# Optimization experiments

Hardware: AMD Instinct MI355X
Metric: run time of the kernel (lower is better)

The kernel has to match this reference:

```python
import jax, jax.numpy as jnp
import numpy as np

HEADS = 16
D_MODEL = 1024
D_K = D_MODEL // HEADS
B, S = 2, 2048
NEG = -1000000000.0


def setup_inputs() -> dict:
    key = jax.random.key(0)
    ks = jax.random.split(key, 8)
    q = jax.random.normal(ks[0], (B, S, D_MODEL), dtype=jnp.float32)
    k = jax.random.normal(ks[1], (B, S, D_MODEL), dtype=jnp.float32)
    v = jax.random.normal(ks[2], (B, S, D_MODEL), dtype=jnp.float32)
    mask = jax.random.randint(ks[3], (B, 1, S, S), 0, 2) > 0  # True = masked
    scale = 1.0 / np.sqrt(D_MODEL)
    Wq = jax.random.normal(ks[4], (D_MODEL, D_MODEL), dtype=jnp.float32) * scale
    Wk = jax.random.normal(ks[5], (D_MODEL, D_MODEL), dtype=jnp.float32) * scale
    Wv = jax.random.normal(ks[6], (D_MODEL, D_MODEL), dtype=jnp.float32) * scale
    Wo = jax.random.normal(ks[7], (D_MODEL, D_MODEL), dtype=jnp.float32) * scale
    return {"q": q, "k": k, "v": v, "mask": mask,
            "Wq": Wq, "Wk": Wk, "Wv": Wv, "Wo": Wo}


def reference(q, k, v, mask, Wq, Wk, Wv, Wo):
    b, s, _ = q.shape
    # torch Linear: x @ W.T ; reshape to [B, H, S, d_k]
    def proj(x, W):
        return (x @ W.T).reshape(b, -1, HEADS, D_K).transpose(0, 2, 1, 3)
    qh, kh, vh = proj(q, Wq), proj(k, Wk), proj(v, Wv)
    # scaled dot-product attention; scale uses d_k (key.shape[-1] after reshape)
    att = jnp.einsum('bhqd,bhkd->bhqk', qh, kh) / jnp.sqrt(jnp.float32(D_K))
    att = jnp.where(mask, NEG, att)
    att = jax.nn.softmax(att, axis=-1)
    out = jnp.einsum('bhqk,bhkd->bhqd', att, vh)  # [B,H,S,d_k]
    out = out.transpose(0, 2, 1, 3).reshape(b, -1, D_MODEL)
    return out @ Wo.T  # dropout is identity at inference
```

## Files before the change

kernel.cpp:

```cpp
#include <hip/hip_runtime.h>

typedef unsigned short u16;
typedef unsigned int   u32;
typedef unsigned char  u8;
typedef unsigned long long u64;
typedef __attribute__((ext_vector_type(8))) short bf16x8;
typedef __attribute__((ext_vector_type(4))) float f32x4;
typedef __attribute__((ext_vector_type(16))) float f32x16;

__device__ __forceinline__ u16 f2b(float f) {
  union { float f; u32 u; } v; v.f = f;
  u32 u = v.u;
  return (u16)((u + 0x7fffu + ((u >> 16) & 1u)) >> 16);
}
__device__ __forceinline__ float b2f(u16 x) {
  union { u32 u; float f; } v; v.u = ((u32)x) << 16; return v.f;
}
__device__ __forceinline__ u32 pk2(u16 lo, u16 hi) { return (u32)lo | ((u32)hi << 16); }

__device__ __forceinline__ float fexp2(float x) { return __builtin_amdgcn_exp2f(x); }

__device__ __forceinline__ u32 cvtpk(float lo, float hi) {
  u32 r;
  asm("v_cvt_pk_bf16_f32 %0, %1, %2" : "=v"(r) : "v"(lo), "v"(hi));
  return r;
}

__device__ __forceinline__ void swap32(u32& a, u32& b) {
  asm("v_permlane32_swap_b32 %0, %1" : "+v"(a), "+v"(b));
}

__device__ __forceinline__ void glds16(const u16* g, u16* l) {
  __builtin_amdgcn_global_load_lds((const __attribute__((address_space(1))) void*)g,
                                   (__attribute__((address_space(3))) void*)l, 16, 0, 0);
}

__global__ __launch_bounds__(256) void mask_detect(const u8* __restrict__ raw,
                                                   int* __restrict__ flag) {
  int i = blockIdx.x * 256 + threadIdx.x;
  uint4 x = ((const uint4*)raw)[i];
  u32 o = x.x | x.y | x.z | x.w;
  u64 b1 = __ballot((o & 0x0000ff00u) != 0);
  u64 b2 = __ballot((o & 0xffff0000u) != 0);
  if ((threadIdx.x & 63) == 0) {
    if (b1) atomicOr(&flag[0], 1);
    if (b2) atomicOr(&flag[1], 1);
  }
}

__global__ __launch_bounds__(256) void mask_bits(const u8* __restrict__ raw,
                                                 u64* __restrict__ out,
                                                 const int* __restrict__ flag) {
  int f = flag[0] ? 2 : (flag[1] ? 1 : 0);
  int i = blockIdx.x * 256 + threadIdx.x;
  bool bit;
  if (f == 2)      bit = raw[i] != 0;
  else if (f == 0) bit = ((const int*)raw)[i] != 0;
  else             bit = ((const float*)raw)[i] != 0.0f;
  u64 b = __ballot(bit);
  if ((threadIdx.x & 63) == 0) out[i >> 6] = b;
}

__global__ __launch_bounds__(256) void conv_w(const float* __restrict__ W0, const float* __restrict__ W1,
                                              const float* __restrict__ W2, const float* __restrict__ W3,
                                              u16* __restrict__ o0, u16* __restrict__ o1,
                                              u16* __restrict__ o2, u16* __restrict__ o3) {
  int zz = blockIdx.z;
  const float* W = zz == 0 ? W0 : zz == 1 ? W1 : zz == 2 ? W2 : W3;
  u16* o = zz == 0 ? o0 : zz == 1 ? o1 : zz == 2 ? o2 : o3;
  int i = (blockIdx.x * 256 + threadIdx.x) * 8;
  float4 a = *(const float4*)(W + i), b2 = *(const float4*)(W + i + 4);
  uint4 t;
  t.x = pk2(f2b(a.x), f2b(a.y));   t.y = pk2(f2b(a.z), f2b(a.w));
  t.z = pk2(f2b(b2.x), f2b(b2.y)); t.w = pk2(f2b(b2.z), f2b(b2.w));
  *(uint4*)(o + i) = t;
}

template<int AF32, int BF32, int CF32>
__device__ __forceinline__ void gemm_body(
    const void* __restrict__ Av, const void* __restrict__ Bv, void* __restrict__ Cv,
    int N, int K, int m0, int n0, float cscale, u16* As, u16* Bs) {
  const int tid = threadIdx.x;
  const int lane = tid & 63, w = tid >> 6;
  const int lr = lane & 15, lg = lane >> 4;
  const int wm = (w >> 1) * 64, wn = (w & 1) * 64;
  const int srow = lane >> 3;
  const int selem = (((lane & 7) ^ srow) << 3);
  const int rsw = (lr & 7) << 3;

  f32x4 acc[4][4];
#pragma unroll
  for (int mi = 0; mi < 4; ++mi)
#pragma unroll
    for (int ni = 0; ni < 4; ++ni)
      acc[mi][ni] = (f32x4){0.f, 0.f, 0.f, 0.f};

  float4 fa0[4], fa1[4], fb0[4], fb1[4];

#define GLDS_SIDE(P, base, k0_, LB)                                            \
  do {                                                                         \
    _Pragma("unroll")                                                          \
    for (int r_ = 0; r_ < 4; ++r_) {                                           \
      const int c_ = w * 4 + r_;                                               \
      const int row_ = c_ * 8 + srow;                                          \
      glds16((const u16*)(P) + (size_t)((base) + row_) * K + (k0_) + selem, (LB) + c_ * 512); \
    }                                                                          \
  } while (0)

#define F32_ISSUE(P, base, k0_, f0, f1)                                        \
  do {                                                                         \
    _Pragma("unroll")                                                          \
    for (int rr = 0; rr < 4; ++rr) {                                           \
      const int ch_ = rr * 256 + tid;                                          \
      const int row_ = ch_ >> 3, col_ = (ch_ & 7) * 8;                         \
      const float* p_ = (const float*)(P) + (size_t)((base) + row_) * K + (k0_) + col_; \
      f0[rr] = *(const float4*)p_;                                             \
      f1[rr] = *(const float4*)(p_ + 4);                                       \
    }                                                                          \
  } while (0)

#define F32_WRITE(LB, f0, f1)                                                  \
  do {                                                                         \
    _Pragma("unroll")                                                          \
    for (int rr = 0; rr < 4; ++rr) {                                           \
      const int ch_ = rr * 256 + tid;                                          \
      const int row_ = ch_ >> 3, col_ = (ch_ & 7) * 8;                         \
      uint4 t_;                                                                \
      t_.x = cvtpk(f0[rr].x, f0[rr].y); t_.y = cvtpk(f0[rr].z, f0[rr].w);      \
      t_.z = cvtpk(f1[rr].x, f1[rr].y); t_.w = cvtpk(f1[rr].z, f1[rr].w);      \
      *(uint4*)&(LB)[row_ * 64 + (col_ ^ ((row_ & 7) << 3))] = t_;             \
    }                                                                          \
  } while (0)

  if (AF32) { F32_ISSUE(Av, m0, 0, fa0, fa1); F32_WRITE(As, fa0, fa1); }
  else      GLDS_SIDE(Av, m0, 0, As);
  if (BF32) { F32_ISSUE(Bv, n0, 0, fb0, fb1); F32_WRITE(Bs, fb0, fb1); }
  else      GLDS_SIDE(Bv, n0, 0, Bs);
  __syncthreads();

  int cur = 0;
  for (int k0 = 0; k0 < K; k0 += 64) {
    const bool nx = (k0 + 64 < K);
    if (nx) {
      if (AF32) F32_ISSUE(Av, m0, k0 + 64, fa0, fa1);
      else      GLDS_SIDE(Av, m0, k0 + 64, As + (cur ^ 1) * 8192);
      if (BF32) F32_ISSUE(Bv, n0, k0 + 64, fb0, fb1);
      else      GLDS_SIDE(Bv, n0, k0 + 64, Bs + (cur ^ 1) * 8192);
    }
    bf16x8 af[4][2], bfv[4][2];
#pragma unroll
    for (int mi = 0; mi < 4; ++mi)
#pragma unroll
      for (int kk = 0; kk < 2; ++kk)
        af[mi][kk] = *(bf16x8*)&As[cur * 8192 + (wm + mi * 16 + lr) * 64 + ((kk * 32 + lg * 8) ^ rsw)];
#pragma unroll
    for (int ni = 0; ni < 4; ++ni)
#pragma unroll
      for (int kk = 0; kk < 2; ++kk)
        bfv[ni][kk] = *(bf16x8*)&Bs[cur * 8192 + (wn + ni * 16 + lr) * 64 + ((kk * 32 + lg * 8) ^ rsw)];
    __builtin_amdgcn_s_setprio(1);
#pragma unroll
    for (int mi = 0; mi < 4; ++mi)
#pragma unroll
      for (int ni = 0; ni < 4; ++ni)
#pragma unroll
        for (int kk = 0; kk < 2; ++kk)
          acc[mi][ni] = __builtin_amdgcn_mfma_f32_16x16x32_bf16(
              af[mi][kk], bfv[ni][kk], acc[mi][ni], 0, 0, 0);
    __builtin_amdgcn_s_setprio(0);
    if (nx) {
      if (AF32) F32_WRITE(As + (cur ^ 1) * 8192, fa0, fa1);
      if (BF32) F32_WRITE(Bs + (cur ^ 1) * 8192, fb0, fb1);
    }
    __syncthreads();
    cur ^= 1;
  }
#undef GLDS_SIDE
#undef F32_ISSUE
#undef F32_WRITE
#pragma unroll
  for (int mi = 0; mi < 4; ++mi)
#pragma unroll
    for (int ni = 0; ni < 4; ++ni)
#pragma unroll
      for (int r = 0; r < 4; ++r) {
        int m = m0 + wm + mi * 16 + lg * 4 + r;
        int n = n0 + wn + ni * 16 + lr;
        float vv = acc[mi][ni][r] * cscale;
        if (CF32) ((float*)Cv)[(size_t)m * N + n] = vv;
        else      ((u16*)Cv)[(size_t)m * N + n] = f2b(vv);
      }
}

__global__ __launch_bounds__(256) void gemm_qkv(
    const float* __restrict__ q, const float* __restrict__ k, const float* __restrict__ v,
    const u16* __restrict__ Wqb, const u16* __restrict__ Wkb, const u16* __restrict__ Wvb,
    u16* __restrict__ Qb, u16* __restrict__ Kb, u16* __restrict__ VTb, float qscale) {
  __shared__ __align__(16) u16 As[2 * 8192];
  __shared__ __align__(16) u16 Bs[2 * 8192];
  const int z = blockIdx.z;
  const int xcd = blockIdx.x & 7, r = blockIdx.x >> 3;
  const int pblk = xcd * 4 + (r & 3);
  const int oblk = r >> 2;
  if (z < 2) {
    const float* act = z ? k : q;
    const u16* Wb = z ? Wkb : Wqb;
    u16* Cb = z ? Kb : Qb;
    gemm_body<1, 0, 0>(act, Wb, Cb, 1024, 1024, pblk * 128, oblk * 128,
                       z ? 1.0f : qscale, As, Bs);
  } else {
    gemm_body<0, 1, 0>(Wvb, v, VTb, 4096, 1024, oblk * 128, pblk * 128, 1.0f, As, Bs);
  }
}

__global__ __launch_bounds__(256) void gemm_o(
    const u16* __restrict__ Ob, const u16* __restrict__ Wob, float* __restrict__ C) {
  __shared__ __align__(16) u16 As[2 * 8192];
  __shared__ __align__(16) u16 Bs[2 * 8192];
  const int idx = blockIdx.x;
  const int xcd = idx & 7, r = idx >> 3;
  const int mblk = xcd * 4 + (r & 3), nblk = r >> 2;
  gemm_body<0, 0, 1>(Ob, Wob, C, 1024, 1024, mblk * 128, nblk * 128, 1.0f, As, Bs);
}

__global__ __launch_bounds__(256, 4) void flash12(const u16* __restrict__ Q,
                                                  const u16* __restrict__ K,
                                                  const u16* __restrict__ VT,
                                                  const u64* __restrict__ mpk,
                                                  u16* __restrict__ O0,
                                                  u16* __restrict__ O1,
                                                  u16* __restrict__ O2,
                                                  float* __restrict__ Lp) {
  __shared__ __align__(16) u16 Ks[2][4096];
  __shared__ __align__(16) u16 Vs[2][4096];
  const int tid = threadIdx.x, lane = tid & 63, w = tid >> 6;
  const int c = lane & 31, h = lane >> 5;
  const int bid = blockIdx.x;
  const int xcd = bid & 7, idx = bid >> 3;
  const int gl = idx >> 4, qblk = idx & 15;
  const int group = xcd * 12 + gl;
  const int split = group % 3;
  const int hb = group / 3;
  const int head = hb & 15, b = hb >> 4;
  const int qw = qblk * 128 + w * 32;
  const int kt0 = (split * 32) / 3;
  const int ktn = ((split + 1) * 32) / 3;
  const int nt = ktn - kt0;
  const size_t kbase = (size_t)b * 2048 * 1024 + (size_t)head * 64;
  const size_t vbase = (size_t)head * 64 * 4096 + (size_t)b * 2048;
  const int srow = lane >> 3;
  const int selem = (((lane & 7) ^ srow) << 3);
  const int rswc = (c & 7) << 3;

  bf16x8 qf[4];
#pragma unroll
  for (int kd = 0; kd < 4; ++kd)
    qf[kd] = *(const bf16x8*)&Q[kbase + (size_t)(qw + c) * 1024 + 16 * kd + 8 * h];

  union { u32 u[4]; bf16x8 v; } ones;
#pragma unroll
  for (int i = 0; i < 4; ++i) ones.u[i] = 0x3f803f80u;

  f32x16 accO0, accO1, accL;
#pragma unroll
  for (int i = 0; i < 16; ++i) { accO0[i] = 0.f; accO1[i] = 0.f; accL[i] = 0.f; }

  const u64* mrp = mpk + ((size_t)b * 2048 + qw + c) * 32;

#define STAGE(buf, t)                                                          \
  do {                                                                         \
    const int k0_ = (t) * 64;                                                  \
    _Pragma("unroll")                                                          \
    for (int r_ = 0; r_ < 2; ++r_) {                                           \
      const int c_ = w * 2 + r_;                                               \
      const int row_ = c_ * 8 + srow;                                          \
      glds16(K + kbase + (size_t)(k0_ + row_) * 1024 + selem, &Ks[buf][c_ * 512]); \
    }                                                                          \
    _Pragma("unroll")                                                          \
    for (int r_ = 0; r_ < 2; ++r_) {                                           \
      const int c_ = w * 2 + r_;                                               \
      const int row_ = c_ * 8 + srow;                                          \
      glds16(VT + vbase + (size_t)row_ * 4096 + k0_ + selem, &Vs[buf][c_ * 512]); \
    }                                                                          \
  } while (0)

  STAGE(0, kt0);
  u64 mb_next = mrp[kt0];
  __syncthreads();

  int cur = 0;
  for (int t = 0; t < nt; ++t) {
    const u64 mb = mb_next;
    if (t + 1 < nt) {
      STAGE(cur ^ 1, kt0 + t + 1);
      mb_next = mrp[kt0 + t + 1];
    }
    const u16* ks = Ks[cur];
    const u16* vs = Vs[cur];
    f32x16 s0, s1;
#pragma unroll
    for (int i = 0; i < 16; ++i) { s0[i] = 0.f; s1[i] = 0.f; }
    __builtin_amdgcn_s_setprio(1);
#pragma unroll
    for (int kd = 0; kd < 4; ++kd) {
      bf16x8 kf0 = *(bf16x8*)&ks[c * 64 + ((16 * kd + 8 * h) ^ rswc)];
      s0 = __builtin_amdgcn_mfma_f32_32x32x16_bf16(kf0, qf[kd], s0, 0, 0, 0);
      bf16x8 kf1 = *(bf16x8*)&ks[(32 + c) * 64 + ((16 * kd + 8 * h) ^ rswc)];
      s1 = __builtin_amdgcn_mfma_f32_32x32x16_bf16(kf1, qf[kd], s1, 0, 0, 0);
    }
    __builtin_amdgcn_s_setprio(0);
    u32 pw[2][4][2];
#pragma unroll
    for (int kb = 0; kb < 2; ++kb) {
      const u32 m32 = (u32)(mb >> (32 * kb + 4 * h));
      float pp[16];
#pragma unroll
      for (int g = 0; g < 4; ++g)
#pragma unroll
        for (int r = 0; r < 4; ++r) {
          float e = fexp2(kb == 0 ? s0[4 * g + r] : s1[4 * g + r]);
          pp[4 * g + r] = ((m32 >> (8 * g + r)) & 1) ? 0.0f : e;
        }
#pragma unroll
      for (int g = 0; g < 4; ++g)
#pragma unroll
        for (int hh = 0; hh < 2; ++hh)
          pw[kb][g][hh] = cvtpk(pp[4 * g + 2 * hh], pp[4 * g + 2 * hh + 1]);
    }
    __builtin_amdgcn_s_setprio(1);
#pragma unroll
    for (int kb = 0; kb < 2; ++kb)
#pragma unroll
      for (int s = 0; s < 2; ++s) {
        u32 w0 = pw[kb][2 * s][0], w2 = pw[kb][2 * s + 1][0];
        swap32(w0, w2);
        u32 w1 = pw[kb][2 * s][1], w3 = pw[kb][2 * s + 1][1];
        swap32(w1, w3);
        union { u32 u[4]; bf16x8 v; } af;
        af.u[0] = w0; af.u[1] = w1; af.u[2] = w2; af.u[3] = w3;
        const int ksg = kb * 2 + s;
        bf16x8 vf0 = *(bf16x8*)&vs[c * 64 + ((16 * ksg + 8 * h) ^ rswc)];
        accO0 = __builtin_amdgcn_mfma_f32_32x32x16_bf16(af.v, vf0, accO0, 0, 0, 0);
        bf16x8 vf1 = *(bf16x8*)&vs[(32 + c) * 64 + ((16 * ksg + 8 * h) ^ rswc)];
        accO1 = __builtin_amdgcn_mfma_f32_32x32x16_bf16(af.v, vf1, accO1, 0, 0, 0);
        accL  = __builtin_amdgcn_mfma_f32_32x32x16_bf16(af.v, ones.v, accL, 0, 0, 0);
      }
    __builtin_amdgcn_s_setprio(0);
    __syncthreads();
    cur ^= 1;
  }
#undef STAGE
  u16* Op = split == 0 ? O0 : split == 1 ? O1 : O2;
  const size_t obase = (size_t)b * 2048 + qw;
#pragma unroll
  for (int g = 0; g < 4; ++g)
#pragma unroll
    for (int r = 0; r < 4; ++r) {
      const int qrow = r + 8 * g + 4 * h;
      const size_t row = obase + qrow;
      const size_t base = row * 1024 + (size_t)head * 64 + c;
      Op[base]      = f2b(accO0[4 * g + r]);
      Op[base + 32] = f2b(accO1[4 * g + r]);
      if (c == 0) Lp[(size_t)split * 65536 + row * 16 + head] = accL[4 * g + r];
    }
}

__global__ __launch_bounds__(256) void combine(const u16* __restrict__ O0,
                                               const u16* __restrict__ O1,
                                               const u16* __restrict__ O2,
                                               const float* __restrict__ Lp,
                                               u16* __restrict__ Ob) {
  int gid = blockIdx.x * 256 + threadIdx.x;
  int row = gid >> 7, chb = (gid & 127) * 8;
  int head = chb >> 6;
  float l = Lp[(size_t)row * 16 + head] + Lp[65536 + (size_t)row * 16 + head] +
            Lp[131072 + (size_t)row * 16 + head];
  float inv = 1.0f / l;
  size_t off = (size_t)row * 1024 + chb;
  union { uint4 q; u16 s[8]; } a, b, c2, o;
  a.q  = *(const uint4*)(O0 + off);
  b.q  = *(const uint4*)(O1 + off);
  c2.q = *(const uint4*)(O2 + off);
#pragma unroll
  for (int j = 0; j < 8; ++j)
    o.s[j] = f2b((b2f(a.s[j]) + b2f(b.s[j]) + b2f(c2.s[j])) * inv);
  *(uint4*)(Ob + off) = o.q;
}

extern "C" void kernel_launch(void* const* d_in, const int* in_sizes, int n_in,
                              void* d_out, int out_size, void* d_ws, size_t ws_size,
                              hipStream_t stream) {
  const float* q    = (const float*)d_in[0];
  const float* k    = (const float*)d_in[1];
  const float* v    = (const float*)d_in[2];
  const u8*    mask = (const u8*)d_in[3];
  const float* Wq   = (const float*)d_in[4];
  const float* Wk   = (const float*)d_in[5];
  const float* Wv   = (const float*)d_in[6];
  const float* Wo   = (const float*)d_in[7];

  u8* ws = (u8*)d_ws;
  int* flag = (int*)ws;
  u64* mpk  = (u64*)(ws + 256);
  u16* Wqb  = (u16*)(ws + 256 + (1u << 20));
  u16* Wkb  = Wqb + (1 << 20);
  u16* Wvb  = Wkb + (1 << 20);
  u16* Wob  = Wvb + (1 << 20);
  const size_t NE = (size_t)4096 * 1024;
  u16* O2   = Wob + (1 << 20);
  u16* Qb   = O2 + NE;
  u16* Kb   = Qb + NE;
  u16* VTb  = Kb + NE;
  u16* O0   = (u16*)d_out;
  u16* O1   = O0 + NE;
  float* Lp = (float*)Wqb;
  u16* Ob   = Qb;

  const float LOG2E = 1.4426950408889634f;

  hipMemsetAsync(flag, 0, 8, stream);
  mask_detect<<<32, 256, 0, stream>>>(mask, flag);
  mask_bits<<<32768, 256, 0, stream>>>(mask, mpk, flag);
  conv_w<<<dim3(512, 1, 4), 256, 0, stream>>>(Wq, Wk, Wv, Wo, Wqb, Wkb, Wvb, Wob);

  gemm_qkv<<<dim3(256, 1, 3), 256, 0, stream>>>(
      q, k, v, Wqb, Wkb, Wvb, Qb, Kb, VTb, 0.125f * LOG2E);

  flash12<<<1536, 256, 0, stream>>>(Qb, Kb, VTb, mpk, O0, O1, O2, Lp);
  combine<<<2048, 256, 0, stream>>>(O0, O1, O2, Lp, Ob);

  gemm_o<<<dim3(256), 256, 0, stream>>>(Ob, Wob, (float*)d_out);
}
```

Baseline: 159.1 us.

## Shrink GEMM tiles to 128x64 single-buffered LDS to double block count

Replaces the 128x128 double-buffered GEMM body with a 128x64 tile body that uses a single LDS buffer, with each wave owning a 32-row slice. Grids for the QKV and output projections double so more blocks fill the 256 CUs, and the smaller LDS and register footprint allows more resident blocks per CU. In exchange, global-to-LDS loads are no longer overlapped with MFMA work inside a block (two barriers per k-step), and operand reuse per block drops.

```diff
diff --git a/kernel.cpp b/kernel.cpp
--- a/kernel.cpp
+++ b/kernel.cpp
@@ -77,40 +77,48 @@
 }
 
 template<int AF32, int BF32, int CF32>
-__device__ __forceinline__ void gemm_body(
+__device__ __forceinline__ void gemm64_body(
     const void* __restrict__ Av, const void* __restrict__ Bv, void* __restrict__ Cv,
     int N, int K, int m0, int n0, float cscale, u16* As, u16* Bs) {
   const int tid = threadIdx.x;
   const int lane = tid & 63, w = tid >> 6;
   const int lr = lane & 15, lg = lane >> 4;
-  const int wm = (w >> 1) * 64, wn = (w & 1) * 64;
+  const int wm = w * 32;
   const int srow = lane >> 3;
   const int selem = (((lane & 7) ^ srow) << 3);
   const int rsw = (lr & 7) << 3;
 
-  f32x4 acc[4][4];
-#pragma unroll
-  for (int mi = 0; mi < 4; ++mi)
+  f32x4 acc[2][4];
+#pragma unroll
+  for (int mi = 0; mi < 2; ++mi)
 #pragma unroll
     for (int ni = 0; ni < 4; ++ni)
       acc[mi][ni] = (f32x4){0.f, 0.f, 0.f, 0.f};
 
-  float4 fa0[4], fa1[4], fb0[4], fb1[4];
-
-#define GLDS_SIDE(P, base, k0_, LB)                                            \
+  float4 fa0[4], fa1[4], fb0[2], fb1[2];
+
+#define GLDS_A(P, k0_)                                                         \
   do {                                                                         \
     _Pragma("unroll")                                                          \
     for (int r_ = 0; r_ < 4; ++r_) {                                           \
       const int c_ = w * 4 + r_;                                               \
       const int row_ = c_ * 8 + srow;                                          \
-      glds16((const u16*)(P) + (size_t)((base) + row_) * K + (k0_) + selem, (LB) + c_ * 512); \
+      glds16((const u16*)(P) + (size_t)(m0 + row_) * K + (k0_) + selem, As + c_ * 512); \
     }                                                                          \
   } while (0)
-
-#define F32_ISSUE(P, base, k0_, f0, f1)                                        \
+#define GLDS_B(P, k0_)                                                         \
   do {                                                                         \
     _Pragma("unroll")                                                          \
-    for (int rr = 0; rr < 4; ++rr) {                                           \
+    for (int r_ = 0; r_ < 2; ++r_) {                                           \
+      const int c_ = w * 2 + r_;                                               \
+      const int row_ = c_ * 8 + srow;                                          \
+      glds16((const u16*)(P) + (size_t)(n0 + row_) * K + (k0_) + selem, Bs + c_ * 512); \
+    }                                                                          \
+  } while (0)
+#define F32_ISSUE(P, base, k0_, f0, f1, NC)                                    \
+  do {                                                                         \
+    _Pragma("unroll")                                                          \
+    for (int rr = 0; rr < (NC); ++rr) {                                        \
       const int ch_ = rr * 256 + tid;                                          \
       const int row_ = ch_ >> 3, col_ = (ch_ & 7) * 8;                         \
       const float* p_ = (const float*)(P) + (size_t)((base) + row_) * K + (k0_) + col_; \
@@ -118,11 +126,10 @@
       f1[rr] = *(const float4*)(p_ + 4);                                       \
     }                                                                          \
   } while (0)
-
-#define F32_WRITE(LB, f0, f1)                                                  \
+#define F32_WRITE(LB, f0, f1, NC)                                              \
   do {                                                                         \
     _Pragma("unroll")                                                          \
-    for (int rr = 0; rr < 4; ++rr) {                                           \
+    for (int rr = 0; rr < (NC); ++rr) {                                        \
       const int ch_ = rr * 256 + tid;                                          \
       const int row_ = ch_ >> 3, col_ = (ch_ & 7) * 8;                         \
       uint4 t_;                                                                \
@@ -132,35 +139,34 @@
     }                                                                          \
   } while (0)
 
-  if (AF32) { F32_ISSUE(Av, m0, 0, fa0, fa1); F32_WRITE(As, fa0, fa1); }
-  else      GLDS_SIDE(Av, m0, 0, As);
-  if (BF32) { F32_ISSUE(Bv, n0, 0, fb0, fb1); F32_WRITE(Bs, fb0, fb1); }
-  else      GLDS_SIDE(Bv, n0, 0, Bs);
-  __syncthreads();
-
-  int cur = 0;
+  if (AF32) F32_ISSUE(Av, m0, 0, fa0, fa1, 4);
+  if (BF32) F32_ISSUE(Bv, n0, 0, fb0, fb1, 2);
   for (int k0 = 0; k0 < K; k0 += 64) {
     const bool nx = (k0 + 64 < K);
+    __syncthreads();
+    if (AF32) F32_WRITE(As, fa0, fa1, 4);
+    else      GLDS_A(Av, k0);
+    if (BF32) F32_WRITE(Bs, fb0, fb1, 2);
+    else      GLDS_B(Bv, k0);
+    __syncthreads();
     if (nx) {
-      if (AF32) F32_ISSUE(Av, m0, k0 + 64, fa0, fa1);
-      else      GLDS_SIDE(Av, m0, k0 + 64, As + (cur ^ 1) * 8192);
-      if (BF32) F32_ISSUE(Bv, n0, k0 + 64, fb0, fb1);
-      else      GLDS_SIDE(Bv, n0, k0 + 64, Bs + (cur ^ 1) * 8192);
+      if (AF32) F32_ISSUE(Av, m0, k0 + 64, fa0, fa1, 4);
+      if (BF32) F32_ISSUE(Bv, n0, k0 + 64, fb0, fb1, 2);
     }
-    bf16x8 af[4][2], bfv[4][2];
-#pragma unroll
-    for (int mi = 0; mi < 4; ++mi)
+    bf16x8 af[2][2], bfv[4][2];
+#pragma unroll
+    for (int mi = 0; mi < 2; ++mi)
 #pragma unroll
       for (int kk = 0; kk < 2; ++kk)
-        af[mi][kk] = *(bf16x8*)&As[cur * 8192 + (wm + mi * 16 + lr) * 64 + ((kk * 32 + lg * 8) ^ rsw)];
+        af[mi][kk] = *(bf16x8*)&As[(wm + mi * 16 + lr) * 64 + ((kk * 32 + lg * 8) ^ rsw)];
 #pragma unroll
     for (int ni = 0; ni < 4; ++ni)
 #pragma unroll
       for (int kk = 0; kk < 2; ++kk)
-        bfv[ni][kk] = *(bf16x8*)&Bs[cur * 8192 + (wn + ni * 16 + lr) * 64 + ((kk * 32 + lg * 8) ^ rsw)];
+        bfv[ni][kk] = *(bf16x8*)&Bs[(ni * 16 + lr) * 64 + ((kk * 32 + lg * 8) ^ rsw)];
     __builtin_amdgcn_s_setprio(1);
 #pragma unroll
-    for (int mi = 0; mi < 4; ++mi)
+    for (int mi = 0; mi < 2; ++mi)
 #pragma unroll
       for (int ni = 0; ni < 4; ++ni)
 #pragma unroll
@@ -168,24 +174,19 @@
           acc[mi][ni] = __builtin_amdgcn_mfma_f32_16x16x32_bf16(
               af[mi][kk], bfv[ni][kk], acc[mi][ni], 0, 0, 0);
     __builtin_amdgcn_s_setprio(0);
-    if (nx) {
-      if (AF32) F32_WRITE(As + (cur ^ 1) * 8192, fa0, fa1);
-      if (BF32) F32_WRITE(Bs + (cur ^ 1) * 8192, fb0, fb1);
-    }
-    __syncthreads();
-    cur ^= 1;
   }
-#undef GLDS_SIDE
+#undef GLDS_A
+#undef GLDS_B
 #undef F32_ISSUE
 #undef F32_WRITE
 #pragma unroll
-  for (int mi = 0; mi < 4; ++mi)
+  for (int mi = 0; mi < 2; ++mi)
 #pragma unroll
     for (int ni = 0; ni < 4; ++ni)
 #pragma unroll
       for (int r = 0; r < 4; ++r) {
         int m = m0 + wm + mi * 16 + lg * 4 + r;
-        int n = n0 + wn + ni * 16 + lr;
+        int n = n0 + ni * 16 + lr;
         float vv = acc[mi][ni][r] * cscale;
         if (CF32) ((float*)Cv)[(size_t)m * N + n] = vv;
         else      ((u16*)Cv)[(size_t)m * N + n] = f2b(vv);
@@ -196,31 +197,33 @@
     const float* __restrict__ q, const float* __restrict__ k, const float* __restrict__ v,
     const u16* __restrict__ Wqb, const u16* __restrict__ Wkb, const u16* __restrict__ Wvb,
     u16* __restrict__ Qb, u16* __restrict__ Kb, u16* __restrict__ VTb, float qscale) {
-  __shared__ __align__(16) u16 As[2 * 8192];
-  __shared__ __align__(16) u16 Bs[2 * 8192];
+  __shared__ __align__(16) u16 As[128 * 64];
+  __shared__ __align__(16) u16 Bs[64 * 64];
   const int z = blockIdx.z;
   const int xcd = blockIdx.x & 7, r = blockIdx.x >> 3;
-  const int pblk = xcd * 4 + (r & 3);
-  const int oblk = r >> 2;
   if (z < 2) {
+    const int pblk = xcd * 4 + (r & 3);
+    const int oblk = r >> 2;
     const float* act = z ? k : q;
     const u16* Wb = z ? Wkb : Wqb;
     u16* Cb = z ? Kb : Qb;
-    gemm_body<1, 0, 0>(act, Wb, Cb, 1024, 1024, pblk * 128, oblk * 128,
-                       z ? 1.0f : qscale, As, Bs);
+    gemm64_body<1, 0, 0>(act, Wb, Cb, 1024, 1024, pblk * 128, oblk * 64,
+                         z ? 1.0f : qscale, As, Bs);
   } else {
-    gemm_body<0, 1, 0>(Wvb, v, VTb, 4096, 1024, oblk * 128, pblk * 128, 1.0f, As, Bs);
+    const int pblk = xcd * 8 + (r & 7);
+    const int oblk = r >> 3;
+    gemm64_body<0, 1, 0>(Wvb, v, VTb, 4096, 1024, oblk * 128, pblk * 64,
+                         1.0f, As, Bs);
   }
 }
 
 __global__ __launch_bounds__(256) void gemm_o(
     const u16* __restrict__ Ob, const u16* __restrict__ Wob, float* __restrict__ C) {
-  __shared__ __align__(16) u16 As[2 * 8192];
-  __shared__ __align__(16) u16 Bs[2 * 8192];
-  const int idx = blockIdx.x;
-  const int xcd = idx & 7, r = idx >> 3;
+  __shared__ __align__(16) u16 As[128 * 64];
+  __shared__ __align__(16) u16 Bs[64 * 64];
+  const int xcd = blockIdx.x & 7, r = blockIdx.x >> 3;
   const int mblk = xcd * 4 + (r & 3), nblk = r >> 2;
-  gemm_body<0, 0, 1>(Ob, Wob, C, 1024, 1024, mblk * 128, nblk * 128, 1.0f, As, Bs);
+  gemm64_body<0, 0, 1>(Ob, Wob, C, 1024, 1024, mblk * 128, nblk * 64, 1.0f, As, Bs);
 }
 
 __global__ __launch_bounds__(256, 4) void flash12(const u16* __restrict__ Q,
@@ -423,11 +426,11 @@
   mask_bits<<<32768, 256, 0, stream>>>(mask, mpk, flag);
   conv_w<<<dim3(512, 1, 4), 256, 0, stream>>>(Wq, Wk, Wv, Wo, Wqb, Wkb, Wvb, Wob);
 
-  gemm_qkv<<<dim3(256, 1, 3), 256, 0, stream>>>(
+  gemm_qkv<<<dim3(512, 1, 3), 256, 0, stream>>>(
       q, k, v, Wqb, Wkb, Wvb, Qb, Kb, VTb, 0.125f * LOG2E);
 
   flash12<<<1536, 256, 0, stream>>>(Qb, Kb, VTb, mpk, O0, O1, O2, Lp);
   combine<<<2048, 256, 0, stream>>>(O0, O1, O2, Lp, Ob);
 
-  gemm_o<<<dim3(256), 256, 0, stream>>>(Ob, Wob, (float*)d_out);
-}
+  gemm_o<<<512, 256, 0, stream>>>(Ob, Wob, (float*)d_out);
+}
```

New measurement: 154.8 us. 2.7% less time.
